# Kernel tuning notes

Measured on AMD Instinct MI355X. Metric: run time of the kernel, lower is better.

## Reference

```python
import jax, jax.numpy as jnp
import numpy as np

N = 300000   # nodes
E = 600000   # edges
H = 128      # hidden_dim
L = 5        # num_layers
G = 8192     # graphs in batch
AV = 128     # atom feature vocab
BV = 8       # bond feature vocab
NAF = 9      # atom int features (OGB)
NBF = 3      # bond int features (OGB)
BN_EPS = 1e-5


def setup_inputs() -> dict:
    key = jax.random.key(0)
    ks = jax.random.split(key, 16)
    s = 0.05
    x = jax.random.randint(ks[0], (N, NAF), 0, 100, dtype=jnp.int32)
    edge_index = jax.random.randint(ks[1], (2, E), 0, N, dtype=jnp.int32)
    edge_attr = jax.random.randint(ks[2], (E, NBF), 0, 6, dtype=jnp.int32)
    batch = jnp.sort(jax.random.randint(ks[3], (N,), 0, G, dtype=jnp.int32))
    atom_emb = jax.random.normal(ks[4], (NAF, AV, H), dtype=jnp.float32) * s
    bond_emb = jax.random.normal(ks[5], (L, NBF, BV, H), dtype=jnp.float32) * s
    eps = jnp.zeros((L,), dtype=jnp.float32)  # GIN train_eps init 0
    w1 = jax.random.normal(ks[6], (L, H, H), dtype=jnp.float32) * s
    b1 = jnp.zeros((L, H), dtype=jnp.float32)
    bn1_g = jnp.ones((L, H), dtype=jnp.float32)
    bn1_b = jnp.zeros((L, H), dtype=jnp.float32)
    w2 = jax.random.normal(ks[7], (L, H, H), dtype=jnp.float32) * s
    b2 = jnp.zeros((L, H), dtype=jnp.float32)
    bn_g = jnp.ones((L, H), dtype=jnp.float32)
    bn_b = jnp.zeros((L, H), dtype=jnp.float32)
    cw1 = jax.random.normal(ks[8], (H, H), dtype=jnp.float32) * s
    cb1 = jnp.zeros((H,), dtype=jnp.float32)
    cw2 = jax.random.normal(ks[9], (H, 1), dtype=jnp.float32) * s
    cb2 = jnp.zeros((1,), dtype=jnp.float32)
    return dict(x=x, edge_index=edge_index, edge_attr=edge_attr, batch=batch,
                atom_emb=atom_emb, bond_emb=bond_emb, eps=eps,
                w1=w1, b1=b1, bn1_g=bn1_g, bn1_b=bn1_b, w2=w2, b2=b2,
                bn_g=bn_g, bn_b=bn_b, cw1=cw1, cb1=cb1, cw2=cw2, cb2=cb2)


def _bn(h, g, b):
    # BatchNorm1d in training mode: biased batch stats over nodes
    mu = h.mean(axis=0)
    var = h.var(axis=0)
    return g * (h - mu) * jax.lax.rsqrt(var + BN_EPS) + b


def reference(x, edge_index, edge_attr, batch, atom_emb, bond_emb, eps,
              w1, b1, bn1_g, bn1_b, w2, b2, bn_g, bn_b, cw1, cb1, cw2, cb2):
    seg = jax.ops.segment_sum
    # AtomEncoder: sum of per-feature embedding lookups -> [N, H]
    h = atom_emb[0][x[:, 0]]
    for f in range(1, NAF):
        h = h + atom_emb[f][x[:, f]]
    row, col = edge_index[0], edge_index[1]
    # in-degree of row used by scatter_reduce_(mean, include_self=True): divide by count+1
    deg = seg(jnp.ones((E,), dtype=h.dtype), row, num_segments=N)
    inv = 1.0 / (deg + 1.0)
    for l in range(L):
        # BondEncoder for this layer -> [E, H]
        be = (bond_emb[l, 0][edge_attr[:, 0]]
              + bond_emb[l, 1][edge_attr[:, 1]]
              + bond_emb[l, 2][edge_attr[:, 2]])
        # scatter mean (include_self=True over initial zeros): sum/(count+1)
        bond_agg = seg(be, row, num_segments=N) * inv[:, None]
        h_in = h + bond_agg
        # GINConv: sum-aggregate source feats at targets, (1+eps)*self + aggr, then MLP
        aggr = seg(h_in[row], col, num_segments=N)
        z = (1.0 + eps[l]) * h_in + aggr
        z = jax.nn.relu(_bn(z @ w1[l] + b1[l], bn1_g[l], bn1_b[l]))
        z = z @ w2[l] + b2[l]
        h = _bn(z, bn_g[l], bn_b[l])
        if l < L - 1:
            h = jax.nn.relu(h)  # dropout p=0 -> identity
    pooled = seg(h, batch, num_segments=G)  # global_add_pool -> [G, H]
    out = jax.nn.relu(pooled @ cw1 + cb1) @ cw2 + cb2  # [G, 1]
    return out.squeeze(-1)
```

## Files before the change

kernel.cpp:

```cpp
#include <hip/hip_runtime.h>
#include <cstdint>

#define NN 300000
#define NE 600000
#define HD 128
#define NL 5
#define NG 8192
#define AVOC 128
#define BVOC 8
#define NAF 9
#define NBF 3
#define BN_EPS 1e-5f

#define SCAN_B 2048
#define SCAN_NB ((NN + SCAN_B - 1) / SCAN_B)

#define G1ROWS 128
#define G1BLK ((NN + G1ROWS - 1) / G1ROWS)
#define GBM 256
#define GBLK ((NN + GBM - 1) / GBM)

typedef unsigned short u16;
typedef unsigned int u32;
typedef __attribute__((ext_vector_type(8))) short bf16x8;
typedef __attribute__((ext_vector_type(4))) float f32x4;

static __device__ __forceinline__ void atomAddF(float* p, float v) { unsafeAtomicAdd(p, v); }

static __device__ __forceinline__ float bf2f(u16 v) {
  union { u32 u; float f; } c; c.u = ((u32)v) << 16; return c.f;
}
static __device__ __forceinline__ u16 f2bf(float f) {
  union { float f; u32 u; } c; c.f = f;
  u32 u = c.u;
  return (u16)((u + 0x7FFFu + ((u >> 16) & 1u)) >> 16);
}
static __device__ __forceinline__ u32 cvtpk(float a, float b) {
  u32 r;
  asm("v_cvt_pk_bf16_f32 %0, %1, %2" : "=v"(r) : "v"(a), "v"(b));
  return r;
}
static __device__ __forceinline__ void unp8(uint4 p, float* v) {
  v[0] = bf2f((u16)(p.x & 0xffff)); v[1] = bf2f((u16)(p.x >> 16));
  v[2] = bf2f((u16)(p.y & 0xffff)); v[3] = bf2f((u16)(p.y >> 16));
  v[4] = bf2f((u16)(p.z & 0xffff)); v[5] = bf2f((u16)(p.z >> 16));
  v[6] = bf2f((u16)(p.w & 0xffff)); v[7] = bf2f((u16)(p.w >> 16));
}
static __device__ __forceinline__ uint4 pk8(const float* v) {
  uint4 p;
  p.x = ((u32)f2bf(v[1]) << 16) | f2bf(v[0]);
  p.y = ((u32)f2bf(v[3]) << 16) | f2bf(v[2]);
  p.z = ((u32)f2bf(v[5]) << 16) | f2bf(v[4]);
  p.w = ((u32)f2bf(v[7]) << 16) | f2bf(v[6]);
  return p;
}

static __device__ __forceinline__ void split8(const float* v, bf16x8& hi, bf16x8& lo) {
  union { u32 u[4]; bf16x8 h; } H, L;
  H.u[0] = cvtpk(v[0], v[1]); H.u[1] = cvtpk(v[2], v[3]);
  H.u[2] = cvtpk(v[4], v[5]); H.u[3] = cvtpk(v[6], v[7]);
  float r[8];
  r[0] = bf2f((u16)(H.u[0] & 0xffff)); r[1] = bf2f((u16)(H.u[0] >> 16));
  r[2] = bf2f((u16)(H.u[1] & 0xffff)); r[3] = bf2f((u16)(H.u[1] >> 16));
  r[4] = bf2f((u16)(H.u[2] & 0xffff)); r[5] = bf2f((u16)(H.u[2] >> 16));
  r[6] = bf2f((u16)(H.u[3] & 0xffff)); r[7] = bf2f((u16)(H.u[3] >> 16));
  L.u[0] = cvtpk(v[0] - r[0], v[1] - r[1]); L.u[1] = cvtpk(v[2] - r[2], v[3] - r[3]);
  L.u[2] = cvtpk(v[4] - r[4], v[5] - r[5]); L.u[3] = cvtpk(v[6] - r[6], v[7] - r[7]);
  hi = H.h; lo = L.h;
}

__global__ __launch_bounds__(256) void count_k(const int* __restrict__ ei,
    int* __restrict__ cnt_row, int* __restrict__ cnt_col) {
  int e = blockIdx.x * 256 + threadIdx.x;
  if (e >= NE) return;
  atomicAdd(&cnt_row[ei[e]], 1);
  atomicAdd(&cnt_col[ei[NE + e]], 1);
}

__global__ __launch_bounds__(256) void scan_block_k(int* __restrict__ P, int* __restrict__ bsum) {
  __shared__ int s[256];
  int b = blockIdx.x, t = threadIdx.x;
  int base = b * SCAN_B + t * 8;
  int v[8]; int ts = 0;
#pragma unroll
  for (int j = 0; j < 8; j++) { v[j] = (base + j < NN) ? P[base + j] : 0; ts += v[j]; }
  s[t] = ts;
  __syncthreads();
  for (int off = 1; off < 256; off <<= 1) {
    int tmp = 0;
    if (t >= off) tmp = s[t - off];
    __syncthreads();
    if (t >= off) s[t] += tmp;
    __syncthreads();
  }
  if (t == 255) bsum[b] = s[255];
  int run = (t == 0) ? 0 : s[t - 1];
#pragma unroll
  for (int j = 0; j < 8; j++) {
    if (base + j < NN) P[base + j] = run;
    run += v[j];
  }
}

__global__ __launch_bounds__(256) void scan_tops_k(int* __restrict__ bsum, int* __restrict__ totOut) {
  __shared__ int s[256];
  int t = threadIdx.x;
  s[t] = (t < SCAN_NB) ? bsum[t] : 0;
  __syncthreads();
  for (int off = 1; off < 256; off <<= 1) {
    int tmp = 0;
    if (t >= off) tmp = s[t - off];
    __syncthreads();
    if (t >= off) s[t] += tmp;
    __syncthreads();
  }
  if (t < SCAN_NB) bsum[t] = (t == 0) ? 0 : s[t - 1];
  if (t == 255) *totOut = s[255];
}

__global__ __launch_bounds__(256) void scan_add_k(int* __restrict__ P, const int* __restrict__ bsum) {
  int b = blockIdx.x, t = threadIdx.x;
  int off = bsum[b];
  int base = b * SCAN_B + t * 8;
#pragma unroll
  for (int j = 0; j < 8; j++)
    if (base + j < NN) P[base + j] += off;
}

__global__ __launch_bounds__(256) void fill_k(const int* __restrict__ ei,
    const int* __restrict__ ptr_row, const int* __restrict__ ptr_col,
    int* __restrict__ fillr, int* __restrict__ fillc,
    int* __restrict__ adj_row, int* __restrict__ adj_col) {
  int e = blockIdx.x * 256 + threadIdx.x;
  if (e >= NE) return;
  int r = ei[e], c = ei[NE + e];
  int p1 = atomicAdd(&fillr[r], 1);
  adj_row[ptr_row[r] + p1] = e;
  int p2 = atomicAdd(&fillc[c], 1);
  adj_col[ptr_col[c] + p2] = r;
}

__global__ __launch_bounds__(256) void inv_k(const int* __restrict__ ptr_row, float* __restrict__ inv) {
  int n = blockIdx.x * 256 + threadIdx.x;
  if (n < NN) inv[n] = 1.0f / ((float)(ptr_row[n + 1] - ptr_row[n]) + 1.0f);
}

__global__ __launch_bounds__(256) void gp_k(const int* __restrict__ batch, int* __restrict__ gp) {
  int g = blockIdx.x * 256 + threadIdx.x;
  if (g > NG) return;
  int lo = 0, hi = NN;
  while (lo < hi) { int mid = (lo + hi) >> 1; if (batch[mid] < g) lo = mid + 1; else hi = mid; }
  gp[g] = lo;
}

__global__ __launch_bounds__(256) void wsplit_k(const float* __restrict__ w1,
    const float* __restrict__ w2, u16* __restrict__ Wt_hi, u16* __restrict__ Wt_lo) {
  int m = blockIdx.x;
  const float* W = (m < NL) ? (w1 + (size_t)m * HD * HD) : (w2 + (size_t)(m - NL) * HD * HD);
  int t = threadIdx.x;
  for (int p = 0; p < 64; p++) {
    int o = p * 256 + t;
    int c = o >> 7, k = o & 127;
    float w = W[k * HD + c];
    u16 hi = f2bf(w);
    float lo = w - bf2f(hi);
    Wt_hi[(size_t)m * HD * HD + o] = hi;
    Wt_lo[(size_t)m * HD * HD + o] = f2bf(lo);
  }
}


template<bool ENC>
__global__ __launch_bounds__(256) void bond_k(const int* __restrict__ ea,
    const float* __restrict__ be, const int* __restrict__ ptr_row,
    const int* __restrict__ adj_row, const float* __restrict__ inv,
    const int* __restrict__ x, const float* __restrict__ emb,
    const u16* __restrict__ Z2, const float* __restrict__ ss,
    u16* __restrict__ A) {
  __shared__ int sx[16 * NAF];
  int t = threadIdx.x;
  int nb = blockIdx.x * 16;
  int n = nb + (t >> 4);
  int c8 = t & 15;
  if constexpr (ENC) {
    if (t < 16 * NAF && nb * NAF + t < NN * NAF) sx[t] = x[nb * NAF + t];
    __syncthreads();
  }
  if (n >= NN) return;
  float h[8];
  if constexpr (ENC) {
#pragma unroll
    for (int j = 0; j < 8; j++) h[j] = 0.f;
#pragma unroll
    for (int f = 0; f < NAF; f++) {
      int v = sx[(t >> 4) * NAF + f];
      const float* e = emb + ((size_t)(f * AVOC + v)) * HD + c8 * 8;
      float4 e0 = *(const float4*)e;
      float4 e1 = *(const float4*)(e + 4);
      h[0] += e0.x; h[1] += e0.y; h[2] += e0.z; h[3] += e0.w;
      h[4] += e1.x; h[5] += e1.y; h[6] += e1.z; h[7] += e1.w;
    }
  } else {
    uint4 p = *(const uint4*)(Z2 + (size_t)n * HD + c8 * 8);
    unp8(p, h);
#pragma unroll
    for (int j = 0; j < 8; j++)
      h[j] = fmaxf(fmaf(h[j], ss[c8 * 8 + j], ss[128 + c8 * 8 + j]), 0.f);
  }
  int beg = ptr_row[n], end = ptr_row[n + 1];
  float acc[8] = {0.f, 0.f, 0.f, 0.f, 0.f, 0.f, 0.f, 0.f};
  for (int i = beg; i < end; i++) {
    int e = adj_row[i];
    int a0 = ea[e * 3 + 0], a1 = ea[e * 3 + 1], a2 = ea[e * 3 + 2];
    const float* p0 = be + (size_t)a0 * HD + c8 * 8;
    const float* p1 = be + (size_t)(BVOC + a1) * HD + c8 * 8;
    const float* p2 = be + (size_t)(2 * BVOC + a2) * HD + c8 * 8;
    float4 x0 = *(const float4*)p0, x1 = *(const float4*)(p0 + 4);
    float4 y0 = *(const float4*)p1, y1 = *(const float4*)(p1 + 4);
    float4 z0 = *(const float4*)p2, z1 = *(const float4*)(p2 + 4);
    acc[0] += x0.x + y0.x + z0.x; acc[1] += x0.y + y0.y + z0.y;
    acc[2] += x0.z + y0.z + z0.z; acc[3] += x0.w + y0.w + z0.w;
    acc[4] += x1.x + y1.x + z1.x; acc[5] += x1.y + y1.y + z1.y;
    acc[6] += x1.z + y1.z + z1.z; acc[7] += x1.w + y1.w + z1.w;
  }
  float iv = inv[n];
#pragma unroll
  for (int j = 0; j < 8; j++) h[j] = fmaf(acc[j], iv, h[j]);
  *(uint4*)(A + (size_t)n * HD + c8 * 8) = pk8(h);
}

__global__ __launch_bounds__(512, 4) void gemm1_aggr_k(
    const u16* __restrict__ A, const int* __restrict__ ptr_col,
    const int* __restrict__ adj_col, const float* __restrict__ eps, int lyr,
    const u16* __restrict__ Whi, const u16* __restrict__ Wlo,
    const float* __restrict__ bias, u16* __restrict__ Z1,
    float* __restrict__ stats) {
  __shared__ u16 sW[2 * HD * HD];
  const int tid = threadIdx.x;
#pragma unroll
  for (int p = 0; p < 4; p++) {
    int idx = tid + p * 512;
    int col = idx >> 4, k16 = idx & 15;
    uint4 vh = *(const uint4*)(Whi + idx * 8);
    uint4 vl = *(const uint4*)(Wlo + idx * 8);
    int so = (col << 7) + ((k16 << 3) ^ ((col & 7) << 3));
    *(uint4*)(sW + so) = vh;
    *(uint4*)(sW + HD * HD + so) = vl;
  }
  __syncthreads();

  const float se = 1.0f + eps[lyr];
  const int l = tid & 63, w = tid >> 6;
  const int lr = l & 15, lk = l >> 4;
  const int rw = blockIdx.x * G1ROWS + w * 16;
  const int gr = rw + lr;
  const int kb0 = lk * 8;

  float z[4][8];
#pragma unroll
  for (int ks = 0; ks < 4; ks++)
#pragma unroll
    for (int j = 0; j < 8; j++) z[ks][j] = 0.f;

  if (gr < NN) {
    const u16* ap = A + (size_t)gr * HD + kb0;
    uint4 s0 = *(const uint4*)(ap);
    uint4 s1 = *(const uint4*)(ap + 32);
    uint4 s2 = *(const uint4*)(ap + 64);
    uint4 s3 = *(const uint4*)(ap + 96);
    int beg = ptr_col[gr], end = ptr_col[gr + 1];
    {
      float v[8];
      unp8(s0, v);
#pragma unroll
      for (int j = 0; j < 8; j++) z[0][j] = v[j] * se;
      unp8(s1, v);
#pragma unroll
      for (int j = 0; j < 8; j++) z[1][j] = v[j] * se;
      unp8(s2, v);
#pragma unroll
      for (int j = 0; j < 8; j++) z[2][j] = v[j] * se;
      unp8(s3, v);
#pragma unroll
      for (int j = 0; j < 8; j++) z[3][j] = v[j] * se;
    }
    if (beg < end) {
      int src = adj_col[beg];
      for (int e = beg; e < end; e++) {
        const u16* sp = A + (size_t)src * HD + kb0;
        uint4 q0 = *(const uint4*)(sp);
        uint4 q1 = *(const uint4*)(sp + 32);
        uint4 q2 = *(const uint4*)(sp + 64);
        uint4 q3 = *(const uint4*)(sp + 96);
        if (e + 1 < end) src = adj_col[e + 1];
        float u[8];
        unp8(q0, u);
#pragma unroll
        for (int j = 0; j < 8; j++) z[0][j] += u[j];
        unp8(q1, u);
#pragma unroll
        for (int j = 0; j < 8; j++) z[1][j] += u[j];
        unp8(q2, u);
#pragma unroll
        for (int j = 0; j < 8; j++) z[2][j] += u[j];
        unp8(q3, u);
#pragma unroll
        for (int j = 0; j < 8; j++) z[3][j] += u[j];
      }
    }
  }

  bf16x8 ah[4], al[4];
#pragma unroll
  for (int ks = 0; ks < 4; ks++) split8(z[ks], ah[ks], al[ks]);

  f32x4 acc[8];
#pragma unroll
  for (int jt = 0; jt < 8; jt++) acc[jt] = (f32x4){0.f, 0.f, 0.f, 0.f};
#pragma unroll
  for (int ks = 0; ks < 4; ks++) {
    const int kb = ks * 32 + kb0;
#pragma unroll
    for (int jt = 0; jt < 8; jt++) {
      int col = jt * 16 + lr;
      int so = (col << 7) + (kb ^ ((col & 7) << 3));
      bf16x8 bh = *(const bf16x8*)(sW + so);
      bf16x8 bl = *(const bf16x8*)(sW + HD * HD + so);
      acc[jt] = __builtin_amdgcn_mfma_f32_16x16x32_bf16(ah[ks], bh, acc[jt], 0, 0, 0);
      acc[jt] = __builtin_amdgcn_mfma_f32_16x16x32_bf16(al[ks], bh, acc[jt], 0, 0, 0);
      acc[jt] = __builtin_amdgcn_mfma_f32_16x16x32_bf16(ah[ks], bl, acc[jt], 0, 0, 0);
    }
  }

  float bb[8];
#pragma unroll
  for (int jt = 0; jt < 8; jt++) bb[jt] = bias[jt * 16 + lr];
  float cs[8], cq[8];
#pragma unroll
  for (int jt = 0; jt < 8; jt++) { cs[jt] = 0.f; cq[jt] = 0.f; }
#pragma unroll
  for (int j = 0; j < 4; j++) {
    int gr2 = rw + lk * 4 + j;
    bool ok = gr2 < NN;
#pragma unroll
    for (int jt = 0; jt < 8; jt++) {
      float o = acc[jt][j] + bb[jt];
      if (ok) { cs[jt] += o; cq[jt] += o * o; }
      float on = __shfl_xor(o, 1);
      u32 pw = cvtpk(o, on);
      if (ok && !(l & 1))
        *(u32*)(Z1 + (size_t)gr2 * HD + jt * 16 + lr) = pw;
    }
  }
#pragma unroll
  for (int jt = 0; jt < 8; jt++) {
    cs[jt] += __shfl_xor(cs[jt], 16); cs[jt] += __shfl_xor(cs[jt], 32);
    cq[jt] += __shfl_xor(cq[jt], 16); cq[jt] += __shfl_xor(cq[jt], 32);
  }
  __syncthreads();
  float* sS = (float*)sW;
  if (lk == 0) {
#pragma unroll
    for (int jt = 0; jt < 8; jt++) {
      sS[w * HD + jt * 16 + lr] = cs[jt];
      sS[1024 + w * HD + jt * 16 + lr] = cq[jt];
    }
  }
  __syncthreads();
  if (tid < HD) {
    float s = 0.f, q = 0.f;
#pragma unroll
    for (int g = 0; g < 8; g++) { s += sS[g * HD + tid]; q += sS[1024 + g * HD + tid]; }
    atomAddF(&stats[tid], s);
    atomAddF(&stats[HD + tid], q);
  }
}

__global__ __launch_bounds__(512, 4) void gemm2_k(
    const u16* __restrict__ Z1, const float* __restrict__ ss,
    const u16* __restrict__ Whi, const u16* __restrict__ Wlo,
    const float* __restrict__ bias, u16* __restrict__ Z2,
    float* __restrict__ stats) {
  __shared__ u16 sW[2 * HD * HD];
  const int tid = threadIdx.x;
#pragma unroll
  for (int p = 0; p < 4; p++) {
    int idx = tid + p * 512;
    int col = idx >> 4, k16 = idx & 15;
    uint4 vh = *(const uint4*)(Whi + idx * 8);
    uint4 vl = *(const uint4*)(Wlo + idx * 8);
    int so = (col << 7) + ((k16 << 3) ^ ((col & 7) << 3));
    *(uint4*)(sW + so) = vh;
    *(uint4*)(sW + HD * HD + so) = vl;
  }
  __syncthreads();

  const int l = tid & 63, w = tid >> 6;
  const int lr = l & 15, lk = l >> 4;
  const int rw = blockIdx.x * GBM + w * 32;
  f32x4 acc[2][8];
#pragma unroll
  for (int i = 0; i < 2; i++)
#pragma unroll
    for (int j = 0; j < 8; j++) acc[i][j] = (f32x4){0.f, 0.f, 0.f, 0.f};

#pragma unroll
  for (int ks = 0; ks < 4; ks++) {
    const int kb = ks * 32 + lk * 8;
    bf16x8 ah[2], al[2];
#pragma unroll
    for (int i = 0; i < 2; i++) {
      int gr = rw + i * 16 + lr;
      uint4 p = make_uint4(0u, 0u, 0u, 0u);
      if (gr < NN) p = *(const uint4*)(Z1 + (size_t)gr * HD + kb);
      float v[8]; unp8(p, v);
#pragma unroll
      for (int j = 0; j < 8; j++)
        v[j] = fmaxf(fmaf(v[j], ss[kb + j], ss[HD + kb + j]), 0.f);
      split8(v, ah[i], al[i]);
    }
#pragma unroll
    for (int jt = 0; jt < 8; jt++) {
      int col = jt * 16 + lr;
      int so = (col << 7) + (kb ^ ((col & 7) << 3));
      bf16x8 bh = *(const bf16x8*)(sW + so);
      bf16x8 bl = *(const bf16x8*)(sW + HD * HD + so);
#pragma unroll
      for (int i = 0; i < 2; i++) {
        acc[i][jt] = __builtin_amdgcn_mfma_f32_16x16x32_bf16(ah[i], bh, acc[i][jt], 0, 0, 0);
        acc[i][jt] = __builtin_amdgcn_mfma_f32_16x16x32_bf16(al[i], bh, acc[i][jt], 0, 0, 0);
        acc[i][jt] = __builtin_amdgcn_mfma_f32_16x16x32_bf16(ah[i], bl, acc[i][jt], 0, 0, 0);
      }
    }
  }

  float bb[8];
#pragma unroll
  for (int jt = 0; jt < 8; jt++) bb[jt] = bias[jt * 16 + lr];
  float cs[8], cq[8];
#pragma unroll
  for (int jt = 0; jt < 8; jt++) { cs[jt] = 0.f; cq[jt] = 0.f; }
#pragma unroll
  for (int i = 0; i < 2; i++)
#pragma unroll
    for (int j = 0; j < 4; j++) {
      int gr = rw + i * 16 + lk * 4 + j;
      bool ok = gr < NN;
#pragma unroll
      for (int jt = 0; jt < 8; jt++) {
        float o = acc[i][jt][j] + bb[jt];
        if (ok) { cs[jt] += o; cq[jt] += o * o; }
        float on = __shfl_xor(o, 1);
        u32 pw = cvtpk(o, on);
        if (ok && !(l & 1))
          *(u32*)(Z2 + (size_t)gr * HD + jt * 16 + lr) = pw;
      }
    }
#pragma unroll
  for (int jt = 0; jt < 8; jt++) {
    cs[jt] += __shfl_xor(cs[jt], 16); cs[jt] += __shfl_xor(cs[jt], 32);
    cq[jt] += __shfl_xor(cq[jt], 16); cq[jt] += __shfl_xor(cq[jt], 32);
  }
  __syncthreads();
  float* sS = (float*)sW;
  if (lk == 0) {
#pragma unroll
    for (int jt = 0; jt < 8; jt++) {
      sS[w * HD + jt * 16 + lr] = cs[jt];
      sS[1024 + w * HD + jt * 16 + lr] = cq[jt];
    }
  }
  __syncthreads();
  if (tid < HD) {
    float s = 0.f, q = 0.f;
#pragma unroll
    for (int g = 0; g < 8; g++) { s += sS[g * HD + tid]; q += sS[1024 + g * HD + tid]; }
    atomAddF(&stats[tid], s);
    atomAddF(&stats[HD + tid], q);
  }
}

__global__ __launch_bounds__(128) void scale_shift_k(float* __restrict__ stats,
    const float* __restrict__ g, const float* __restrict__ b) {
  int c = threadIdx.x;
  float mean = stats[c] * (1.0f / NN);
  float var = stats[HD + c] * (1.0f / NN) - mean * mean;
  float sc = g[c] * rsqrtf(var + BN_EPS);
  stats[256 + c] = sc;
  stats[384 + c] = fmaf(-mean, sc, b[c]);
}

__global__ __launch_bounds__(128) void pool_final_k(const u16* __restrict__ Z2,
    const float* __restrict__ ss, const int* __restrict__ gp,
    const float* __restrict__ cw1, const float* __restrict__ cb1,
    const float* __restrict__ cw2, const float* __restrict__ cb2,
    float* __restrict__ out) {
  __shared__ float sp[128];
  __shared__ float sh[128];
  int g = blockIdx.x, t = threadIdx.x;
  int beg = gp[g], end = gp[g + 1];
  float acc = 0.f;
  for (int n = beg; n < end; n++) acc += bf2f(Z2[(size_t)n * HD + t]);
  sp[t] = fmaf(acc, ss[t], (float)(end - beg) * ss[128 + t]);
  __syncthreads();
  float h1 = cb1[t];
#pragma unroll
  for (int k = 0; k < HD; k++) h1 = fmaf(sp[k], cw1[k * HD + t], h1);
  h1 = fmaxf(h1, 0.f);
  sh[t] = h1 * cw2[t];
  __syncthreads();
  for (int s = 64; s >= 1; s >>= 1) {
    if (t < s) sh[t] += sh[t + s];
    __syncthreads();
  }
  if (t == 0) out[g] = sh[0] + cb2[0];
}

extern "C" void kernel_launch(void* const* d_in, const int* in_sizes, int n_in,
                              void* d_out, int out_size, void* d_ws, size_t ws_size,
                              hipStream_t stream) {
  const int*   x        = (const int*)d_in[0];
  const int*   ei       = (const int*)d_in[1];
  const int*   ea       = (const int*)d_in[2];
  const int*   batch    = (const int*)d_in[3];
  const float* atom_emb = (const float*)d_in[4];
  const float* bond_emb = (const float*)d_in[5];
  const float* eps      = (const float*)d_in[6];
  const float* w1       = (const float*)d_in[7];
  const float* b1       = (const float*)d_in[8];
  const float* bn1_g    = (const float*)d_in[9];
  const float* bn1_b    = (const float*)d_in[10];
  const float* w2       = (const float*)d_in[11];
  const float* b2       = (const float*)d_in[12];
  const float* bn_g     = (const float*)d_in[13];
  const float* bn_b     = (const float*)d_in[14];
  const float* cw1      = (const float*)d_in[15];
  const float* cb1      = (const float*)d_in[16];
  const float* cw2      = (const float*)d_in[17];
  const float* cb2      = (const float*)d_in[18];
  float* out = (float*)d_out;

  const size_t NH = (size_t)NN * HD;
  float* ws = (float*)d_ws;
  float* stats   = ws;
  int*   ptr_row = (int*)(ws + 5 * 1024);
  int*   ptr_col = ptr_row + (NN + 1);
  int*   adj_row = ptr_col + (NN + 1);
  int*   adj_col = adj_row + NE;
  int*   gp      = adj_col + NE;
  float* inv     = (float*)(gp + (NG + 1));
  size_t off = 5 * 1024 + 2 * (size_t)(NN + 1) + 2 * (size_t)NE + (NG + 1) + NN;
  off = (off + 3) & ~(size_t)3;
  float* B = ws + off;
  u16*   Z1 = (u16*)B;
  u16*   Z2 = Z1 + NH;
  u16*   A  = (u16*)(B + NH);
  u16*   Wt_hi = A + NH;
  u16*   Wt_lo = Wt_hi + 10 * HD * HD;
  int* fillr = (int*)B;
  int* fillc = fillr + NN;
  int* bsums = fillc + NN;

  const int nb_node = (NN + 15) / 16;
  const int nb_e    = (NE + 255) / 256;

  hipMemsetAsync(stats, 0, 5 * 1024 * sizeof(float), stream);
  hipMemsetAsync(ptr_row, 0, 2 * (NN + 1) * sizeof(int), stream);
  hipMemsetAsync(fillr, 0, 2 * NN * sizeof(int), stream);

  count_k<<<nb_e, 256, 0, stream>>>(ei, ptr_row, ptr_col);
  scan_block_k<<<SCAN_NB, 256, 0, stream>>>(ptr_row, bsums);
  scan_tops_k<<<1, 256, 0, stream>>>(bsums, &ptr_row[NN]);
  scan_add_k<<<SCAN_NB, 256, 0, stream>>>(ptr_row, bsums);
  scan_block_k<<<SCAN_NB, 256, 0, stream>>>(ptr_col, bsums);
  scan_tops_k<<<1, 256, 0, stream>>>(bsums, &ptr_col[NN]);
  scan_add_k<<<SCAN_NB, 256, 0, stream>>>(ptr_col, bsums);
  inv_k<<<(NN + 255) / 256, 256, 0, stream>>>(ptr_row, inv);
  fill_k<<<nb_e, 256, 0, stream>>>(ei, ptr_row, ptr_col, fillr, fillc, adj_row, adj_col);
  wsplit_k<<<2 * NL, 256, 0, stream>>>(w1, w2, Wt_hi, Wt_lo);
  gp_k<<<(NG + 1 + 255) / 256, 256, 0, stream>>>(batch, gp);

  for (int l = 0; l < NL; l++) {
    const float* be = bond_emb + (size_t)l * NBF * BVOC * HD;
    float* st = stats + (size_t)l * 1024;
    if (l == 0) {
      bond_k<true><<<nb_node, 256, 0, stream>>>(ea, be, ptr_row, adj_row, inv,
          x, atom_emb, nullptr, nullptr, A);
    } else {
      bond_k<false><<<nb_node, 256, 0, stream>>>(ea, be, ptr_row, adj_row, inv,
          nullptr, nullptr, Z2, stats + (size_t)(l - 1) * 1024 + 768, A);
    }
    gemm1_aggr_k<<<G1BLK, 512, 0, stream>>>(A, ptr_col, adj_col, eps, l,
        Wt_hi + (size_t)l * HD * HD, Wt_lo + (size_t)l * HD * HD,
        b1 + (size_t)l * HD, Z1, st);
    scale_shift_k<<<1, 128, 0, stream>>>(st, bn1_g + (size_t)l * HD, bn1_b + (size_t)l * HD);
    gemm2_k<<<GBLK, 512, 0, stream>>>(Z1, st + 256,
        Wt_hi + (size_t)(NL + l) * HD * HD, Wt_lo + (size_t)(NL + l) * HD * HD,
        b2 + (size_t)l * HD, Z2, st + 512);
    scale_shift_k<<<1, 128, 0, stream>>>(st + 512, bn_g + (size_t)l * HD, bn_b + (size_t)l * HD);
  }

  pool_final_k<<<NG, 128, 0, stream>>>(Z2, stats + 4 * 1024 + 768, gp,
      cw1, cb1, cw2, cb2, out);
}
```

Measured before the change: 1.562 ms.

## Precombine bond embedding triples into a table and store packed codes in CSR

Builds a per-layer table of all 512 combinations of the three bond-feature embeddings. The row-CSR now stores a 16-bit packed bond code per edge instead of an edge id, so the bond aggregation does one indirect load and one table row read per edge. The previous path needed an edge id, three attribute loads and three embedding row reads. This adds a small precompute kernel and about 1.3 MB of table, and the CSR loop also prefetches the next code early.

```diff
diff --git a/kernel.cpp b/kernel.cpp
--- a/kernel.cpp
+++ b/kernel.cpp
@@ -128,14 +128,16 @@
 }
 
 __global__ __launch_bounds__(256) void fill_k(const int* __restrict__ ei,
+    const int* __restrict__ ea,
     const int* __restrict__ ptr_row, const int* __restrict__ ptr_col,
     int* __restrict__ fillr, int* __restrict__ fillc,
-    int* __restrict__ adj_row, int* __restrict__ adj_col) {
+    u16* __restrict__ adjc, int* __restrict__ adj_col) {
   int e = blockIdx.x * 256 + threadIdx.x;
   if (e >= NE) return;
   int r = ei[e], c = ei[NE + e];
+  int a0 = ea[e * 3 + 0], a1 = ea[e * 3 + 1], a2 = ea[e * 3 + 2];
   int p1 = atomicAdd(&fillr[r], 1);
-  adj_row[ptr_row[r] + p1] = e;
+  adjc[ptr_row[r] + p1] = (u16)(a0 + (a1 << 3) + (a2 << 6));
   int p2 = atomicAdd(&fillc[c], 1);
   adj_col[ptr_col[c] + p2] = r;
 }
@@ -169,11 +171,22 @@
   }
 }
 
+__global__ __launch_bounds__(128) void cmb_k(const float* __restrict__ bond_emb,
+    float* __restrict__ cmb) {
+  int b = blockIdx.x;
+  int l = b >> 9, c = b & 511;
+  int t = threadIdx.x;
+  const float* be = bond_emb + (size_t)l * NBF * BVOC * HD;
+  float v = be[(c & 7) * HD + t] + be[(BVOC + ((c >> 3) & 7)) * HD + t]
+          + be[(2 * BVOC + (c >> 6)) * HD + t];
+  cmb[(size_t)b * HD + t] = v;
+}
+
 
 template<bool ENC>
-__global__ __launch_bounds__(256) void bond_k(const int* __restrict__ ea,
-    const float* __restrict__ be, const int* __restrict__ ptr_row,
-    const int* __restrict__ adj_row, const float* __restrict__ inv,
+__global__ __launch_bounds__(256) void bond_k(
+    const float* __restrict__ cmb, const int* __restrict__ ptr_row,
+    const u16* __restrict__ adjc, const float* __restrict__ inv,
     const int* __restrict__ x, const float* __restrict__ emb,
     const u16* __restrict__ Z2, const float* __restrict__ ss,
     u16* __restrict__ A) {
@@ -187,6 +200,19 @@
     __syncthreads();
   }
   if (n >= NN) return;
+  int beg = ptr_row[n], end = ptr_row[n + 1];
+  float acc[8] = {0.f, 0.f, 0.f, 0.f, 0.f, 0.f, 0.f, 0.f};
+  if (beg < end) {
+    int c = adjc[beg];
+    for (int i = beg; i < end; i++) {
+      const float* p = cmb + ((size_t)c << 7) + c8 * 8;
+      float4 x0 = *(const float4*)p;
+      float4 x1 = *(const float4*)(p + 4);
+      if (i + 1 < end) c = adjc[i + 1];
+      acc[0] += x0.x; acc[1] += x0.y; acc[2] += x0.z; acc[3] += x0.w;
+      acc[4] += x1.x; acc[5] += x1.y; acc[6] += x1.z; acc[7] += x1.w;
+    }
+  }
   float h[8];
   if constexpr (ENC) {
 #pragma unroll
@@ -206,22 +232,6 @@
 #pragma unroll
     for (int j = 0; j < 8; j++)
       h[j] = fmaxf(fmaf(h[j], ss[c8 * 8 + j], ss[128 + c8 * 8 + j]), 0.f);
-  }
-  int beg = ptr_row[n], end = ptr_row[n + 1];
-  float acc[8] = {0.f, 0.f, 0.f, 0.f, 0.f, 0.f, 0.f, 0.f};
-  for (int i = beg; i < end; i++) {
-    int e = adj_row[i];
-    int a0 = ea[e * 3 + 0], a1 = ea[e * 3 + 1], a2 = ea[e * 3 + 2];
-    const float* p0 = be + (size_t)a0 * HD + c8 * 8;
-    const float* p1 = be + (size_t)(BVOC + a1) * HD + c8 * 8;
-    const float* p2 = be + (size_t)(2 * BVOC + a2) * HD + c8 * 8;
-    float4 x0 = *(const float4*)p0, x1 = *(const float4*)(p0 + 4);
-    float4 y0 = *(const float4*)p1, y1 = *(const float4*)(p1 + 4);
-    float4 z0 = *(const float4*)p2, z1 = *(const float4*)(p2 + 4);
-    acc[0] += x0.x + y0.x + z0.x; acc[1] += x0.y + y0.y + z0.y;
-    acc[2] += x0.z + y0.z + z0.z; acc[3] += x0.w + y0.w + z0.w;
-    acc[4] += x1.x + y1.x + z1.x; acc[5] += x1.y + y1.y + z1.y;
-    acc[6] += x1.z + y1.z + z1.z; acc[7] += x1.w + y1.w + z1.w;
   }
   float iv = inv[n];
 #pragma unroll
@@ -545,8 +555,8 @@
   float* stats   = ws;
   int*   ptr_row = (int*)(ws + 5 * 1024);
   int*   ptr_col = ptr_row + (NN + 1);
-  int*   adj_row = ptr_col + (NN + 1);
-  int*   adj_col = adj_row + NE;
+  u16*   adjc    = (u16*)(ptr_col + (NN + 1));
+  int*   adj_col = (int*)adjc + NE;
   int*   gp      = adj_col + NE;
   float* inv     = (float*)(gp + (NG + 1));
   size_t off = 5 * 1024 + 2 * (size_t)(NN + 1) + 2 * (size_t)NE + (NG + 1) + NN;
@@ -557,6 +567,7 @@
   u16*   A  = (u16*)(B + NH);
   u16*   Wt_hi = A + NH;
   u16*   Wt_lo = Wt_hi + 10 * HD * HD;
+  float* cmb   = (float*)(Wt_lo + 10 * HD * HD);
   int* fillr = (int*)B;
   int* fillc = fillr + NN;
   int* bsums = fillc + NN;
@@ -576,18 +587,19 @@
   scan_tops_k<<<1, 256, 0, stream>>>(bsums, &ptr_col[NN]);
   scan_add_k<<<SCAN_NB, 256, 0, stream>>>(ptr_col, bsums);
   inv_k<<<(NN + 255) / 256, 256, 0, stream>>>(ptr_row, inv);
-  fill_k<<<nb_e, 256, 0, stream>>>(ei, ptr_row, ptr_col, fillr, fillc, adj_row, adj_col);
+  fill_k<<<nb_e, 256, 0, stream>>>(ei, ea, ptr_row, ptr_col, fillr, fillc, adjc, adj_col);
   wsplit_k<<<2 * NL, 256, 0, stream>>>(w1, w2, Wt_hi, Wt_lo);
+  cmb_k<<<NL * 512, 128, 0, stream>>>(bond_emb, cmb);
   gp_k<<<(NG + 1 + 255) / 256, 256, 0, stream>>>(batch, gp);
 
   for (int l = 0; l < NL; l++) {
-    const float* be = bond_emb + (size_t)l * NBF * BVOC * HD;
+    const float* cl = cmb + (size_t)l * 512 * HD;
     float* st = stats + (size_t)l * 1024;
     if (l == 0) {
-      bond_k<true><<<nb_node, 256, 0, stream>>>(ea, be, ptr_row, adj_row, inv,
+      bond_k<true><<<nb_node, 256, 0, stream>>>(cl, ptr_row, adjc, inv,
           x, atom_emb, nullptr, nullptr, A);
     } else {
-      bond_k<false><<<nb_node, 256, 0, stream>>>(ea, be, ptr_row, adj_row, inv,
+      bond_k<false><<<nb_node, 256, 0, stream>>>(cl, ptr_row, adjc, inv,
           nullptr, nullptr, Z2, stats + (size_t)(l - 1) * 1024 + 768, A);
     }
     gemm1_aggr_k<<<G1BLK, 512, 0, stream>>>(A, ptr_col, adj_col, eps, l,
```

Result: faster. 1.371 ms (-12.2%).
